# Kernel optimization log

Hardware: AMD Instinct MI355X
Metric: run time of the kernel (lower is better)

Reference implementation:

```python
import jax, jax.numpy as jnp
import numpy as np

B, N, D = 32, 1024, 512
NUM_CLASSES = 4
LN_EPS = 1e-5


def _layer_norm(x, g, b):
    mu = jnp.mean(x, axis=-1, keepdims=True)
    var = jnp.mean(jnp.square(x - mu), axis=-1, keepdims=True)
    return (x - mu) * jax.lax.rsqrt(var + LN_EPS) * g + b


def setup_inputs() -> dict:
    key = jax.random.key(0)
    ks = jax.random.split(key, 8)
    s = 0.05
    inp = {
        "sc_matrix": jax.random.uniform(ks[0], (B, N, N), dtype=jnp.float32),
        # GCN encoder params
        "W1": jax.random.normal(ks[1], (N, D), dtype=jnp.float32) * s,
        "b1": jnp.zeros((D,), jnp.float32),
        "W2": jax.random.normal(ks[2], (D, D), dtype=jnp.float32) * s,
        "b2": jnp.zeros((D,), jnp.float32),
        "ln_g": jnp.ones((D,), jnp.float32),
        "ln_b": jnp.zeros((D,), jnp.float32),
        # classifier params
        "Wc1": jax.random.normal(ks[3], (D, 128), dtype=jnp.float32) * s,
        "bc1": jnp.zeros((128,), jnp.float32),
        "g1": jnp.ones((128,), jnp.float32),
        "t1": jnp.zeros((128,), jnp.float32),
        "Wc2": jax.random.normal(ks[4], (128, 64), dtype=jnp.float32) * s,
        "bc2": jnp.zeros((64,), jnp.float32),
        "g2": jnp.ones((64,), jnp.float32),
        "t2": jnp.zeros((64,), jnp.float32),
        "Wc3": jax.random.normal(ks[5], (64, NUM_CLASSES), dtype=jnp.float32) * s,
        "bc3": jnp.zeros((NUM_CLASSES,), jnp.float32),
    }
    return inp


def reference(sc_matrix, W1, b1, W2, b2, ln_g, ln_b,
              Wc1, bc1, g1, t1, Wc2, bc2, g2, t2, Wc3, bc3):
    # Every entry of sc_matrix is nonzero, so the edge list covers all (i,j)
    # pairs incl. self-loops; GCN message passing == dense normalized matmul.
    # PyG gcn_norm: deg[j] = sum_i A[i,j]; out = D^-1/2 A^T D^-1/2 h.
    A = sc_matrix                              # [B,N,N], A[b,i,j] = edge i->j
    deg = jnp.sum(A, axis=-2)                  # col sums, [B,N]
    dis = jnp.where(deg > 0, jax.lax.rsqrt(deg), 0.0)   # deg^{-1/2}
    An = jnp.swapaxes(A, -1, -2) * dis[:, :, None] * dis[:, None, :]  # [B,N,N]

    x = sc_matrix                              # node features = SC rows [B,N,N]
    h = jax.nn.relu(jnp.matmul(An, jnp.matmul(x, W1)) + b1)   # conv1+relu [B,N,D]
    h = jnp.matmul(An, jnp.matmul(h, W2)) + b2                # conv2      [B,N,D]
    z = _layer_norm(h, ln_g, ln_b)

    z_pooled = jnp.mean(z, axis=1)             # [B,D]

    c = jax.nn.relu(_layer_norm(z_pooled @ Wc1 + bc1, g1, t1))
    c = jax.nn.relu(_layer_norm(c @ Wc2 + bc2, g2, t2))
    logits = c @ Wc3 + bc3                     # [B,num_classes]
    return (logits, z_pooled)
```

## Files before the change

### kernel.cpp

```cpp
#include <hip/hip_runtime.h>
#include <hip/hip_bf16.h>

#define B_ 32
#define N_ 1024
#define D_ 512
#define LN_EPS 1e-5f

using bf16 = __bf16;
using bf16x4 = __attribute__((ext_vector_type(4))) __bf16;
using bf16x8 = __attribute__((ext_vector_type(8))) __bf16;
using floatx4 = __attribute__((ext_vector_type(4))) float;

__device__ __forceinline__ void gld16(const bf16* gp, bf16* lp) {
  __builtin_amdgcn_global_load_lds(
      (const __attribute__((address_space(1))) void*)gp,
      (__attribute__((address_space(3))) void*)lp, 16, 0, 0);
}

__global__ __launch_bounds__(256) void k_deg(const float* __restrict__ A,
                                             float* __restrict__ deg,
                                             bf16* __restrict__ Abf) {
  int b = blockIdx.y;
  int i0 = blockIdx.x * 32;
  int t = threadIdx.x;
  const float* p = A + (size_t)b * N_ * N_ + (size_t)i0 * N_ + t * 4;
  bf16* op = Abf + (size_t)b * N_ * N_ + (size_t)i0 * N_ + t * 4;
  float4 acc = {0.f, 0.f, 0.f, 0.f};
  #pragma unroll 4
  for (int i = 0; i < 32; ++i) {
    float4 v = *(const float4*)(p + (size_t)i * N_);
    acc.x += v.x; acc.y += v.y; acc.z += v.z; acc.w += v.w;
    bf16x4 o = {(bf16)v.x, (bf16)v.y, (bf16)v.z, (bf16)v.w};
    *(bf16x4*)(op + (size_t)i * N_) = o;
  }
  float* d = deg + b * N_ + t * 4;
  atomicAdd(d + 0, acc.x); atomicAdd(d + 1, acc.y);
  atomicAdd(d + 2, acc.z); atomicAdd(d + 3, acc.w);
}

__global__ __launch_bounds__(256) void k_build(const bf16* __restrict__ Abf,
                                               const float* __restrict__ deg,
                                               bf16* __restrict__ Anbf) {
  __shared__ float tile[64][65];
  __shared__ float disI[64], disJ[64];
  int b = blockIdx.z;
  int i0 = blockIdx.x * 64;
  int j0 = blockIdx.y * 64;
  int t = threadIdx.x;
  const bf16* Ab = Abf + (size_t)b * N_ * N_;
  bf16* Anb = Anbf + (size_t)b * N_ * N_;
  if (t < 64) {
    float v = deg[b * N_ + i0 + t];
    disI[t] = v > 0.f ? rsqrtf(v) : 0.f;
  } else if (t < 128) {
    float v = deg[b * N_ + j0 + (t - 64)];
    disJ[t - 64] = v > 0.f ? rsqrtf(v) : 0.f;
  }
  #pragma unroll
  for (int cc = 0; cc < 4; ++cc) {
    int chunk = cc * 256 + t;
    int r = chunk >> 4;
    int c4 = (chunk & 15) << 2;
    bf16x4 v = *(const bf16x4*)(Ab + (size_t)(j0 + r) * N_ + i0 + c4);
    tile[r][c4 + 0] = (float)v[0]; tile[r][c4 + 1] = (float)v[1];
    tile[r][c4 + 2] = (float)v[2]; tile[r][c4 + 3] = (float)v[3];
  }
  __syncthreads();
  #pragma unroll
  for (int cc = 0; cc < 4; ++cc) {
    int chunk = cc * 256 + t;
    int ii = chunk >> 4;
    int jj4 = (chunk & 15) << 2;
    float di = disI[ii];
    bf16x4 o;
    #pragma unroll
    for (int e = 0; e < 4; ++e)
      o[e] = (bf16)(tile[jj4 + e][ii] * di * disJ[jj4 + e]);
    *(bf16x4*)(Anb + (size_t)(i0 + ii) * N_ + j0 + jj4) = o;
  }
}

__global__ __launch_bounds__(256) void k_transpose(const float* __restrict__ W1,
                                                   bf16* __restrict__ W1t,
                                                   const float* __restrict__ W2,
                                                   bf16* __restrict__ W2t) {
  __shared__ float tile[64][65];
  int blk = blockIdx.x;
  const float* in; bf16* outp; int R, C, c0, r0;
  if (blk < 128) {
    in = W1; outp = W1t; R = N_; C = D_;
    c0 = (blk & 7) * 64; r0 = (blk >> 3) * 64;
  } else {
    blk -= 128;
    in = W2; outp = W2t; R = D_; C = D_;
    c0 = (blk & 7) * 64; r0 = (blk >> 3) * 64;
  }
  int t = threadIdx.x;
  #pragma unroll
  for (int cc = 0; cc < 4; ++cc) {
    int idx = cc * 256 + t;
    int r = idx >> 4, c4 = (idx & 15) << 2;
    const float4 v = *(const float4*)(in + (size_t)(r0 + r) * C + c0 + c4);
    tile[r][c4 + 0] = v.x; tile[r][c4 + 1] = v.y;
    tile[r][c4 + 2] = v.z; tile[r][c4 + 3] = v.w;
  }
  __syncthreads();
  #pragma unroll
  for (int cc = 0; cc < 4; ++cc) {
    int idx = cc * 256 + t;
    int c = idx >> 4, r4 = (idx & 15) << 2;
    bf16* dst = outp + (size_t)(c0 + c) * R + r0 + r4;
    #pragma unroll
    for (int e = 0; e < 4; ++e) dst[e] = (bf16)tile[r4 + e][c];
  }
}

template <bool BIAS, bool RELU>
__global__ __launch_bounds__(256, 4) void k_gemm(
    const bf16* __restrict__ Abase, size_t strideA,
    const bf16* __restrict__ Btbase, size_t strideBt,
    bf16* __restrict__ Cbase, size_t strideC,
    const float* __restrict__ bias, int Nn, int K) {
  __shared__ bf16 sA[128 * 64];
  __shared__ bf16 sB[128 * 64];
  int nxy = gridDim.x * gridDim.y;
  int L = blockIdx.z * nxy + blockIdx.y * gridDim.x + blockIdx.x;
  int b = (L & 7) + 8 * (L / (nxy * 8));
  int inner = (L >> 3) % nxy;
  int n0 = (inner % gridDim.x) * 128;
  int m0 = (inner / gridDim.x) * 128;

  const bf16* A = Abase + (size_t)b * strideA;
  const bf16* Bt = Btbase + (size_t)b * strideBt;
  int t = threadIdx.x;
  int lane = t & 63, wid = t >> 6;
  int wm = (wid >> 1) * 64, wn = (wid & 1) * 64;
  int l16 = lane & 15, q = lane >> 4;

  int rowoff = lane >> 3;
  int schunk = (lane & 7) ^ rowoff;
  const bf16* agp = A + (size_t)(m0 + wid * 32 + rowoff) * K + schunk * 8;
  const bf16* bgp = Bt + (size_t)(n0 + wid * 32 + rowoff) * K + schunk * 8;
  bf16* alp = &sA[wid * 2048 + lane * 8];
  bf16* blp = &sB[wid * 2048 + lane * 8];

  int xorb = l16 & 7;

  floatx4 acc[4][4];
  #pragma unroll
  for (int i = 0; i < 4; ++i)
    #pragma unroll
    for (int j = 0; j < 4; ++j) acc[i][j] = (floatx4){0.f, 0.f, 0.f, 0.f};

  for (int kt = 0; kt < K; kt += 64) {
    #pragma unroll
    for (int s = 0; s < 4; ++s) {
      gld16(agp + (size_t)s * 8 * K + kt, alp + s * 512);
      gld16(bgp + (size_t)s * 8 * K + kt, blp + s * 512);
    }
    __syncthreads();
    #pragma unroll
    for (int h = 0; h < 2; ++h) {
      int cko = ((q + 4 * h) ^ xorb) * 8;
      bf16x8 af[4], bfr[4];
      #pragma unroll
      for (int mt = 0; mt < 4; ++mt)
        af[mt] = *(const bf16x8*)(&sA[(wm + mt * 16 + l16) * 64 + cko]);
      #pragma unroll
      for (int nt = 0; nt < 4; ++nt)
        bfr[nt] = *(const bf16x8*)(&sB[(wn + nt * 16 + l16) * 64 + cko]);
      #pragma unroll
      for (int mt = 0; mt < 4; ++mt)
        #pragma unroll
        for (int nt = 0; nt < 4; ++nt)
          acc[mt][nt] = __builtin_amdgcn_mfma_f32_16x16x32_bf16(
              af[mt], bfr[nt], acc[mt][nt], 0, 0, 0);
    }
    __syncthreads();
  }

  bf16* C = Cbase + (size_t)b * strideC;
  #pragma unroll
  for (int mt = 0; mt < 4; ++mt)
    #pragma unroll
    for (int nt = 0; nt < 4; ++nt)
      #pragma unroll
      for (int r = 0; r < 4; ++r) {
        int row = m0 + wm + mt * 16 + q * 4 + r;
        int col = n0 + wn + nt * 16 + l16;
        float v = acc[mt][nt][r];
        if (BIAS) v += bias[col];
        if (RELU) v = v > 0.f ? v : 0.f;
        C[(size_t)row * Nn + col] = (bf16)v;
      }
}

__global__ __launch_bounds__(256) void k_lnpool(const bf16* __restrict__ H2,
                                                const float* __restrict__ g,
                                                const float* __restrict__ be,
                                                float* __restrict__ zp_accum) {
  int b = blockIdx.y;
  int r0 = blockIdx.x * 64;
  int t = threadIdx.x, lane = t & 63, w = t >> 6;
  float ge[8], bee[8];
  #pragma unroll
  for (int e = 0; e < 8; ++e) { ge[e] = g[lane * 8 + e]; bee[e] = be[lane * 8 + e]; }
  float acc[8] = {0, 0, 0, 0, 0, 0, 0, 0};
  for (int rr = 0; rr < 16; ++rr) {
    int row = r0 + w * 16 + rr;
    const bf16* p = H2 + ((size_t)b * N_ + row) * D_ + lane * 8;
    bf16x8 hv = *(const bf16x8*)p;
    float x[8];
    float s = 0.f;
    #pragma unroll
    for (int e = 0; e < 8; ++e) { x[e] = (float)hv[e]; s += x[e]; }
    #pragma unroll
    for (int off = 32; off; off >>= 1) s += __shfl_xor(s, off);
    float mu = s * (1.f / 512.f);
    float ss = 0.f;
    #pragma unroll
    for (int e = 0; e < 8; ++e) { float d = x[e] - mu; ss += d * d; }
    #pragma unroll
    for (int off = 32; off; off >>= 1) ss += __shfl_xor(ss, off);
    float rs = rsqrtf(ss * (1.f / 512.f) + LN_EPS);
    #pragma unroll
    for (int e = 0; e < 8; ++e) acc[e] += (x[e] - mu) * rs * ge[e] + bee[e];
  }
  __shared__ float part[4][512];
  #pragma unroll
  for (int e = 0; e < 8; ++e) part[w][lane * 8 + e] = acc[e];
  __syncthreads();
  #pragma unroll
  for (int k = 0; k < 2; ++k) {
    int d = t + k * 256;
    float s4 = part[0][d] + part[1][d] + part[2][d] + part[3][d];
    atomicAdd(&zp_accum[b * D_ + d], s4);
  }
}

__global__ __launch_bounds__(128) void k_cls(
    const float* __restrict__ zp_accum,
    const float* __restrict__ Wc1, const float* __restrict__ bc1,
    const float* __restrict__ g1, const float* __restrict__ t1,
    const float* __restrict__ Wc2, const float* __restrict__ bc2,
    const float* __restrict__ g2, const float* __restrict__ t2,
    const float* __restrict__ Wc3, const float* __restrict__ bc3,
    float* __restrict__ out) {
  __shared__ float z[512];
  __shared__ float c1s[128];
  __shared__ float c2s[64];
  __shared__ float red[128];
  int b = blockIdx.x, t = threadIdx.x;
  #pragma unroll
  for (int k = 0; k < 4; ++k) {
    int d = t + k * 128;
    float v = zp_accum[b * 512 + d] * (1.f / 1024.f);
    z[d] = v;
    out[128 + b * 512 + d] = v;
  }
  __syncthreads();
  float y = bc1[t];
  for (int d = 0; d < 512; ++d) y += z[d] * Wc1[d * 128 + t];
  red[t] = y;
  __syncthreads();
  float mu = 0.f;
  for (int k = 0; k < 128; ++k) mu += red[k];
  mu *= (1.f / 128.f);
  float var = 0.f;
  for (int k = 0; k < 128; ++k) { float dd = red[k] - mu; var += dd * dd; }
  var *= (1.f / 128.f);
  float c = (y - mu) * rsqrtf(var + LN_EPS) * g1[t] + t1[t];
  c1s[t] = c > 0.f ? c : 0.f;
  __syncthreads();
  if (t < 64) {
    float y2 = bc2[t];
    for (int k = 0; k < 128; ++k) y2 += c1s[k] * Wc2[k * 64 + t];
    red[t] = y2;
  }
  __syncthreads();
  if (t < 64) {
    float mu2 = 0.f;
    for (int k = 0; k < 64; ++k) mu2 += red[k];
    mu2 *= (1.f / 64.f);
    float v2 = 0.f;
    for (int k = 0; k < 64; ++k) { float dd = red[k] - mu2; v2 += dd * dd; }
    v2 *= (1.f / 64.f);
    float cc = (red[t] - mu2) * rsqrtf(v2 + LN_EPS) * g2[t] + t2[t];
    c2s[t] = cc > 0.f ? cc : 0.f;
  }
  __syncthreads();
  if (t < 4) {
    float y3 = bc3[t];
    for (int k = 0; k < 64; ++k) y3 += c2s[k] * Wc3[k * 4 + t];
    out[b * 4 + t] = y3;
  }
}

extern "C" void kernel_launch(void* const* d_in, const int* in_sizes, int n_in,
                              void* d_out, int out_size, void* d_ws, size_t ws_size,
                              hipStream_t stream) {
  const float* A   = (const float*)d_in[0];
  const float* W1  = (const float*)d_in[1];
  const float* b1  = (const float*)d_in[2];
  const float* W2  = (const float*)d_in[3];
  const float* b2  = (const float*)d_in[4];
  const float* lng = (const float*)d_in[5];
  const float* lnb = (const float*)d_in[6];
  const float* Wc1 = (const float*)d_in[7];
  const float* bc1 = (const float*)d_in[8];
  const float* g1  = (const float*)d_in[9];
  const float* t1  = (const float*)d_in[10];
  const float* Wc2 = (const float*)d_in[11];
  const float* bc2 = (const float*)d_in[12];
  const float* g2  = (const float*)d_in[13];
  const float* t2  = (const float*)d_in[14];
  const float* Wc3 = (const float*)d_in[15];
  const float* bc3 = (const float*)d_in[16];
  float* out = (float*)d_out;

  char* ws = (char*)d_ws;
  size_t off = 0;
  auto alloc = [&](size_t bytes) {
    char* p = ws + off;
    off += (bytes + 255) & ~(size_t)255;
    return p;
  };
  float* deg  = (float*)alloc((size_t)B_ * N_ * 4);
  float* zp   = (float*)alloc((size_t)B_ * D_ * 4);
  bf16* Anbf  = (bf16*)alloc((size_t)B_ * N_ * N_ * 2);
  bf16* W1t   = (bf16*)alloc((size_t)D_ * N_ * 2);
  bf16* W2t   = (bf16*)alloc((size_t)D_ * D_ * 2);
  bf16* T12t  = (bf16*)alloc((size_t)B_ * D_ * N_ * 2);
  bf16* H1    = (bf16*)alloc((size_t)B_ * N_ * D_ * 2);
  bf16* Abf   = (bf16*)alloc((size_t)B_ * N_ * N_ * 2);
  bf16* H2    = Abf;

  hipMemsetAsync(deg, 0, (size_t)B_ * N_ * 4 + (size_t)B_ * D_ * 4 + 256, stream);

  k_deg<<<dim3(32, B_), 256, 0, stream>>>(A, deg, Abf);
  k_build<<<dim3(16, 16, B_), 256, 0, stream>>>(Abf, deg, Anbf);
  k_transpose<<<192, 256, 0, stream>>>(W1, W1t, W2, W2t);

  k_gemm<false, false><<<dim3(8, 4, B_), 256, 0, stream>>>(
      W1t, 0, Abf, (size_t)N_ * N_, T12t, (size_t)D_ * N_, nullptr, N_, N_);
  k_gemm<true, true><<<dim3(4, 8, B_), 256, 0, stream>>>(
      Anbf, (size_t)N_ * N_, T12t, (size_t)D_ * N_, H1, (size_t)N_ * D_, b1, D_, N_);
  k_gemm<false, false><<<dim3(8, 4, B_), 256, 0, stream>>>(
      W2t, 0, H1, (size_t)N_ * D_, T12t, (size_t)D_ * N_, nullptr, N_, D_);
  k_gemm<true, false><<<dim3(4, 8, B_), 256, 0, stream>>>(
      Anbf, (size_t)N_ * N_, T12t, (size_t)D_ * N_, H2, (size_t)N_ * D_, b2, D_, N_);

  k_lnpool<<<dim3(16, B_), 256, 0, stream>>>(H2, lng, lnb, zp);
  k_cls<<<B_, 128, 0, stream>>>(zp, Wc1, bc1, g1, t1, Wc2, bc2, g2, t2, Wc3, bc3, out);
}
```

Before: 426.4 us.

## Double-buffer GEMM LDS tiles with K=32 prefetch and fold weight transpose into build

The GEMM main loop changes from a single 64-wide K tile with two barriers per step to two 32-wide LDS buffers. The next tile is issued via global_load_lds right after the barrier, so the loads overlap with MFMA work on the current buffer. The LDS swizzle is redone for the 32-element row width. Separately, the W1/W2 transpose is folded into the normalized-adjacency build kernel as an extra grid slice, which removes one launch. The tradeoff is twice as many loop iterations, each with less work to hide latency behind, and the prefetch only helps if the barrier does not already force load completion.

```diff
diff --git a/kernel.cpp b/kernel.cpp
--- a/kernel.cpp
+++ b/kernel.cpp
@@ -40,13 +40,48 @@
 
 __global__ __launch_bounds__(256) void k_build(const bf16* __restrict__ Abf,
                                                const float* __restrict__ deg,
-                                               bf16* __restrict__ Anbf) {
+                                               bf16* __restrict__ Anbf,
+                                               const float* __restrict__ W1,
+                                               bf16* __restrict__ W1t,
+                                               const float* __restrict__ W2,
+                                               bf16* __restrict__ W2t) {
   __shared__ float tile[64][65];
+  int t = threadIdx.x;
+  if (blockIdx.z == 32) {
+    int blk = blockIdx.y * 16 + blockIdx.x;
+    if (blk >= 192) return;
+    const float* in; bf16* outp; int R, C, c0, r0;
+    if (blk < 128) {
+      in = W1; outp = W1t; R = N_; C = D_;
+      c0 = (blk & 7) * 64; r0 = (blk >> 3) * 64;
+    } else {
+      blk -= 128;
+      in = W2; outp = W2t; R = D_; C = D_;
+      c0 = (blk & 7) * 64; r0 = (blk >> 3) * 64;
+    }
+    #pragma unroll
+    for (int cc = 0; cc < 4; ++cc) {
+      int idx = cc * 256 + t;
+      int r = idx >> 4, c4 = (idx & 15) << 2;
+      const float4 v = *(const float4*)(in + (size_t)(r0 + r) * C + c0 + c4);
+      tile[r][c4 + 0] = v.x; tile[r][c4 + 1] = v.y;
+      tile[r][c4 + 2] = v.z; tile[r][c4 + 3] = v.w;
+    }
+    __syncthreads();
+    #pragma unroll
+    for (int cc = 0; cc < 4; ++cc) {
+      int idx = cc * 256 + t;
+      int c = idx >> 4, r4 = (idx & 15) << 2;
+      bf16* dst = outp + (size_t)(c0 + c) * R + r0 + r4;
+      #pragma unroll
+      for (int e = 0; e < 4; ++e) dst[e] = (bf16)tile[r4 + e][c];
+    }
+    return;
+  }
   __shared__ float disI[64], disJ[64];
   int b = blockIdx.z;
   int i0 = blockIdx.x * 64;
   int j0 = blockIdx.y * 64;
-  int t = threadIdx.x;
   const bf16* Ab = Abf + (size_t)b * N_ * N_;
   bf16* Anb = Anbf + (size_t)b * N_ * N_;
   if (t < 64) {
@@ -80,49 +115,14 @@
   }
 }
 
-__global__ __launch_bounds__(256) void k_transpose(const float* __restrict__ W1,
-                                                   bf16* __restrict__ W1t,
-                                                   const float* __restrict__ W2,
-                                                   bf16* __restrict__ W2t) {
-  __shared__ float tile[64][65];
-  int blk = blockIdx.x;
-  const float* in; bf16* outp; int R, C, c0, r0;
-  if (blk < 128) {
-    in = W1; outp = W1t; R = N_; C = D_;
-    c0 = (blk & 7) * 64; r0 = (blk >> 3) * 64;
-  } else {
-    blk -= 128;
-    in = W2; outp = W2t; R = D_; C = D_;
-    c0 = (blk & 7) * 64; r0 = (blk >> 3) * 64;
-  }
-  int t = threadIdx.x;
-  #pragma unroll
-  for (int cc = 0; cc < 4; ++cc) {
-    int idx = cc * 256 + t;
-    int r = idx >> 4, c4 = (idx & 15) << 2;
-    const float4 v = *(const float4*)(in + (size_t)(r0 + r) * C + c0 + c4);
-    tile[r][c4 + 0] = v.x; tile[r][c4 + 1] = v.y;
-    tile[r][c4 + 2] = v.z; tile[r][c4 + 3] = v.w;
-  }
-  __syncthreads();
-  #pragma unroll
-  for (int cc = 0; cc < 4; ++cc) {
-    int idx = cc * 256 + t;
-    int c = idx >> 4, r4 = (idx & 15) << 2;
-    bf16* dst = outp + (size_t)(c0 + c) * R + r0 + r4;
-    #pragma unroll
-    for (int e = 0; e < 4; ++e) dst[e] = (bf16)tile[r4 + e][c];
-  }
-}
-
 template <bool BIAS, bool RELU>
 __global__ __launch_bounds__(256, 4) void k_gemm(
     const bf16* __restrict__ Abase, size_t strideA,
     const bf16* __restrict__ Btbase, size_t strideBt,
     bf16* __restrict__ Cbase, size_t strideC,
     const float* __restrict__ bias, int Nn, int K) {
-  __shared__ bf16 sA[128 * 64];
-  __shared__ bf16 sB[128 * 64];
+  __shared__ alignas(16) bf16 sA[2][128 * 32];
+  __shared__ alignas(16) bf16 sB[2][128 * 32];
   int nxy = gridDim.x * gridDim.y;
   int L = blockIdx.z * nxy + blockIdx.y * gridDim.x + blockIdx.x;
   int b = (L & 7) + 8 * (L / (nxy * 8));
@@ -137,14 +137,12 @@
   int wm = (wid >> 1) * 64, wn = (wid & 1) * 64;
   int l16 = lane & 15, q = lane >> 4;
 
-  int rowoff = lane >> 3;
-  int schunk = (lane & 7) ^ rowoff;
-  const bf16* agp = A + (size_t)(m0 + wid * 32 + rowoff) * K + schunk * 8;
-  const bf16* bgp = Bt + (size_t)(n0 + wid * 32 + rowoff) * K + schunk * 8;
-  bf16* alp = &sA[wid * 2048 + lane * 8];
-  bf16* blp = &sB[wid * 2048 + lane * 8];
-
-  int xorb = l16 & 7;
+  int rl = lane >> 2;
+  int g = (lane & 3) ^ ((lane >> 3) & 3);
+  const bf16* agp = A + (size_t)(m0 + wid * 32 + rl) * K + g * 8;
+  const bf16* bgp = Bt + (size_t)(n0 + wid * 32 + rl) * K + g * 8;
+
+  int cko = ((q ^ ((l16 >> 1) & 3))) * 8;
 
   floatx4 acc[4][4];
   #pragma unroll
@@ -152,31 +150,36 @@
     #pragma unroll
     for (int j = 0; j < 4; ++j) acc[i][j] = (floatx4){0.f, 0.f, 0.f, 0.f};
 
-  for (int kt = 0; kt < K; kt += 64) {
-    #pragma unroll
-    for (int s = 0; s < 4; ++s) {
-      gld16(agp + (size_t)s * 8 * K + kt, alp + s * 512);
-      gld16(bgp + (size_t)s * 8 * K + kt, blp + s * 512);
-    }
+  auto stage = [&](int buf, int ko) {
+    bf16* al = &sA[buf][wid * 1024 + lane * 8];
+    bf16* bl = &sB[buf][wid * 1024 + lane * 8];
+    gld16(agp + ko, al);
+    gld16(agp + (size_t)16 * K + ko, al + 512);
+    gld16(bgp + ko, bl);
+    gld16(bgp + (size_t)16 * K + ko, bl + 512);
+  };
+
+  stage(0, 0);
+  #pragma unroll 2
+  for (int kt = 0; kt < K; kt += 32) {
+    int cb = (kt >> 5) & 1;
     __syncthreads();
-    #pragma unroll
-    for (int h = 0; h < 2; ++h) {
-      int cko = ((q + 4 * h) ^ xorb) * 8;
-      bf16x8 af[4], bfr[4];
-      #pragma unroll
-      for (int mt = 0; mt < 4; ++mt)
-        af[mt] = *(const bf16x8*)(&sA[(wm + mt * 16 + l16) * 64 + cko]);
+    if (kt + 32 < K) stage(cb ^ 1, kt + 32);
+    const bf16* sAc = sA[cb];
+    const bf16* sBc = sB[cb];
+    bf16x8 af[4], bfr[4];
+    #pragma unroll
+    for (int mt = 0; mt < 4; ++mt)
+      af[mt] = *(const bf16x8*)(&sAc[(wm + mt * 16 + l16) * 32 + cko]);
+    #pragma unroll
+    for (int nt = 0; nt < 4; ++nt)
+      bfr[nt] = *(const bf16x8*)(&sBc[(wn + nt * 16 + l16) * 32 + cko]);
+    #pragma unroll
+    for (int mt = 0; mt < 4; ++mt)
       #pragma unroll
       for (int nt = 0; nt < 4; ++nt)
-        bfr[nt] = *(const bf16x8*)(&sB[(wn + nt * 16 + l16) * 64 + cko]);
-      #pragma unroll
-      for (int mt = 0; mt < 4; ++mt)
-        #pragma unroll
-        for (int nt = 0; nt < 4; ++nt)
-          acc[mt][nt] = __builtin_amdgcn_mfma_f32_16x16x32_bf16(
-              af[mt], bfr[nt], acc[mt][nt], 0, 0, 0);
-    }
-    __syncthreads();
+        acc[mt][nt] = __builtin_amdgcn_mfma_f32_16x16x32_bf16(
+            af[mt], bfr[nt], acc[mt][nt], 0, 0, 0);
   }
 
   bf16* C = Cbase + (size_t)b * strideC;
@@ -338,8 +341,7 @@
   hipMemsetAsync(deg, 0, (size_t)B_ * N_ * 4 + (size_t)B_ * D_ * 4 + 256, stream);
 
   k_deg<<<dim3(32, B_), 256, 0, stream>>>(A, deg, Abf);
-  k_build<<<dim3(16, 16, B_), 256, 0, stream>>>(Abf, deg, Anbf);
-  k_transpose<<<192, 256, 0, stream>>>(W1, W1t, W2, W2t);
+  k_build<<<dim3(16, 16, 33), 256, 0, stream>>>(Abf, deg, Anbf, W1, W1t, W2, W2t);
 
   k_gemm<false, false><<<dim3(8, 4, B_), 256, 0, stream>>>(
       W1t, 0, Abf, (size_t)N_ * N_, T12t, (size_t)D_ * N_, nullptr, N_, N_);
```

Result: slower. 444.4 us (+4.2%).
